# Kernel tuning notes

Measured on AMD Instinct MI355X. Metric: run time of the kernel, lower is better.

Reference implementation:

```python
import jax, jax.numpy as jnp
import numpy as np

N = 50000
E = 500000
HID = 64
HEADS = 4
LAYERS = 4
CDIM = 8


def _p(key, shape, scale=0.05):
    return jax.random.normal(key, shape, dtype=jnp.float32) * scale


def setup_inputs() -> dict:
    key = jax.random.key(0)
    ks = jax.random.split(key, 32)
    x = jax.random.normal(ks[0], (N, 8), dtype=jnp.float32)
    src = jax.random.randint(ks[1], (E,), 0, N)
    dst = jax.random.randint(ks[2], (E,), 0, N)
    edge_index = jnp.stack([src, dst]).astype(jnp.int64)
    HC = HEADS * HID
    inp = {
        "x": x,
        "edge_index": edge_index,
        # encoder: Linear(8,64), ELU, Linear(64,64), ELU
        "enc_w1": _p(ks[3], (HID, 8)), "enc_b1": _p(ks[4], (HID,)),
        "enc_w2": _p(ks[5], (HID, HID)), "enc_b2": _p(ks[6], (HID,)),
        # per-layer TransformerConv params, stacked over layers
        "Wq": _p(ks[7], (LAYERS, HC, HID)), "bq": _p(ks[8], (LAYERS, HC)),
        "Wk": _p(ks[9], (LAYERS, HC, HID)), "bk": _p(ks[10], (LAYERS, HC)),
        "Wv": _p(ks[11], (LAYERS, HC, HID)), "bv": _p(ks[12], (LAYERS, HC)),
        "Ws": _p(ks[13], (LAYERS, HID, HID)), "bs": _p(ks[14], (LAYERS, HID)),
        # output MLP: 64->64->32->8
        "out_w1": _p(ks[15], (64, HID)), "out_b1": _p(ks[16], (64,)),
        "out_w2": _p(ks[17], (32, 64)), "out_b2": _p(ks[18], (32,)),
        "out_w3": _p(ks[19], (CDIM, 32)), "out_b3": _p(ks[20], (CDIM,)),
    }
    return inp


def transformer_conv(h, src, dst, Wq, bq, Wk, bk, Wv, bv, Ws, bs):
    """PyG TransformerConv, concat=False, root_weight=True, eval mode (no dropout)."""
    n = h.shape[0]
    q = (h @ Wq.T + bq).reshape(n, HEADS, HID)
    k = (h @ Wk.T + bk).reshape(n, HEADS, HID)
    v = (h @ Wv.T + bv).reshape(n, HEADS, HID)
    # per-edge multi-head scores: (E, H)
    alpha = jnp.einsum("ehd,ehd->eh", q[dst], k[src]) / np.sqrt(HID).astype(np.float32)
    # segment softmax over edges grouped by destination node
    amax = jax.ops.segment_max(alpha, dst, num_segments=n)          # (N, H)
    ex = jnp.exp(alpha - amax[dst])                                 # (E, H)
    denom = jax.ops.segment_sum(ex, dst, num_segments=n)           # (N, H)
    w = ex / denom[dst]                                             # (E, H)
    msg = v[src] * w[:, :, None]                                    # (E, H, C)
    agg = jax.ops.segment_sum(msg, dst, num_segments=n)            # (N, H, C)
    out = agg.mean(axis=1)                                          # concat=False -> head mean
    return out + h @ Ws.T + bs                                      # skip connection


def reference(x, edge_index, enc_w1, enc_b1, enc_w2, enc_b2,
              Wq, bq, Wk, bk, Wv, bv, Ws, bs,
              out_w1, out_b1, out_w2, out_b2, out_w3, out_b3):
    src, dst = edge_index[0], edge_index[1]
    elu = jax.nn.elu
    h = elu(x @ enc_w1.T + enc_b1)
    h = elu(h @ enc_w2.T + enc_b2)
    for l in range(LAYERS):
        h = elu(transformer_conv(h, src, dst, Wq[l], bq[l], Wk[l], bk[l],
                                 Wv[l], bv[l], Ws[l], bs[l]))
        # dropout is identity in eval mode
    o = elu(h @ out_w1.T + out_b1)
    o = elu(o @ out_w2.T + out_b2)
    o = o @ out_w3.T + out_b3
    return o
```

## Files before the change

### kernel.cpp

```cpp
#include <hip/hip_runtime.h>
#include <hip/hip_bf16.h>

#define N_NODES 50000
#define N_EDGES 500000
constexpr int HID = 64;
constexpr int HC  = 256;

typedef unsigned short u16;
typedef unsigned char u8;
typedef __attribute__((ext_vector_type(8))) __bf16 bf16x8;
typedef __attribute__((ext_vector_type(4))) float f32x4;
typedef __attribute__((ext_vector_type(2))) float f32x2;

__device__ __forceinline__ float b2f(u16 u) {
    union { unsigned int i; float f; } c; c.i = ((unsigned int)u) << 16; return c.f;
}
__device__ __forceinline__ u16 f2b(float f) {
    union { float f; unsigned int i; } c; c.f = f;
    unsigned int x = c.i;
    unsigned int lsb = (x >> 16) & 1u;
    x += 0x7fffu + lsb;
    return (u16)(x >> 16);
}
__device__ __forceinline__ float elu_f(float x) { return x > 0.f ? x : expm1f(x); }


__global__ __launch_bounds__(256) void init_kernel(int* __restrict__ cnt, int* __restrict__ cursor) {
    int i = blockIdx.x * 256 + threadIdx.x;
    if (i < N_NODES) { cnt[i] = 0; cursor[i] = 0; }
}

__global__ __launch_bounds__(256) void detect_kernel(const int* __restrict__ ei, int* __restrict__ flag) {
    __shared__ int s[4];
    int t = threadIdx.x;
    int nz = ei[2 * t + 1] != 0;
    unsigned long long m = __ballot(nz);
    if ((t & 63) == 0) s[t >> 6] = (m != 0ull) ? 1 : 0;
    __syncthreads();
    if (t == 0) flag[0] = s[0] | s[1] | s[2] | s[3];
}

__global__ __launch_bounds__(256) void wcvt_kernel(const float* __restrict__ Wq, const float* __restrict__ Wk,
                                                   const float* __restrict__ Wv, const float* __restrict__ Wsk,
                                                   u16* __restrict__ w16) {
    int i = blockIdx.x * 256 + threadIdx.x;
    if (i >= 53248) return;
    const float* src; int off;
    if (i < 16384)      { src = Wq;  off = i; }
    else if (i < 32768) { src = Wk;  off = i - 16384; }
    else if (i < 49152) { src = Wv;  off = i - 32768; }
    else                { src = Wsk; off = i - 49152; }
    float4 v = ((const float4*)src)[off];
    ushort4 u; u.x = f2b(v.x); u.y = f2b(v.y); u.z = f2b(v.z); u.w = f2b(v.w);
    ((ushort4*)w16)[i] = u;
}

__global__ __launch_bounds__(256) void hist_kernel(const int* __restrict__ ei, const int* __restrict__ flag,
                                                   int* __restrict__ cnt) {
    int e = blockIdx.x * 256 + threadIdx.x;
    if (e < N_EDGES) {
        int d = flag[0] ? ei[N_EDGES + e] : ei[2 * N_EDGES + 2 * e];
        atomicAdd(&cnt[d], 1);
    }
}

__global__ __launch_bounds__(512) void scan1_kernel(const int* __restrict__ cnt,
                                                    int* __restrict__ row_start, int* __restrict__ bsum) {
    __shared__ int sc[512];
    int t = threadIdx.x;
    int i = blockIdx.x * 512 + t;
    int v = (i < N_NODES) ? cnt[i] : 0;
    sc[t] = v;
    __syncthreads();
    for (int off = 1; off < 512; off <<= 1) {
        int u = (t >= off) ? sc[t - off] : 0;
        __syncthreads();
        sc[t] += u;
        __syncthreads();
    }
    if (i < N_NODES) row_start[i] = sc[t] - v;
    if (t == 511) bsum[blockIdx.x] = sc[511];
}

__global__ __launch_bounds__(128) void scan2_kernel(int* __restrict__ bsum, int* __restrict__ row_start) {
    __shared__ int sc[128];
    const int NB = (N_NODES + 511) / 512;
    int t = threadIdx.x;
    int v = (t < NB) ? bsum[t] : 0;
    sc[t] = v;
    __syncthreads();
    for (int off = 1; off < 128; off <<= 1) {
        int u = (t >= off) ? sc[t - off] : 0;
        __syncthreads();
        sc[t] += u;
        __syncthreads();
    }
    if (t < NB) bsum[t] = sc[t] - v;
    if (t == 127) row_start[N_NODES] = sc[127];
}

__global__ __launch_bounds__(512) void scan3_kernel(int* __restrict__ row_start, const int* __restrict__ bsum) {
    int i = blockIdx.x * 512 + threadIdx.x;
    if (i < N_NODES) row_start[i] += bsum[blockIdx.x];
}

__global__ __launch_bounds__(256) void scatter_kernel(const int* __restrict__ ei, const int* __restrict__ flag,
                                const int* __restrict__ row_start, int* __restrict__ cursor,
                                int* __restrict__ csr_src) {
    int e = blockIdx.x * 256 + threadIdx.x;
    if (e < N_EDGES) {
        int isI32 = flag[0];
        int s = isI32 ? ei[e] : ei[2 * e];
        int d = isI32 ? ei[N_EDGES + e] : ei[2 * N_EDGES + 2 * e];
        int pos = row_start[d] + atomicAdd(&cursor[d], 1);
        csr_src[pos] = s;
    }
}

__global__ __launch_bounds__(256) void encoder_kernel(const float* __restrict__ x,
                               const float* __restrict__ w1, const float* __restrict__ b1,
                               const float* __restrict__ w2, const float* __restrict__ b2,
                               float* __restrict__ h) {
    __shared__ float xs[64 * 9];
    __shared__ float w1s[64 * 9];
    __shared__ u16 t1s[64 * 72];
    __shared__ u16 w2s[64 * 72];
    __shared__ float b1s[64], b2s[64];
    int t = threadIdx.x;
    int m0 = blockIdx.x * 64;

    if (t < 128) {
        int row = t >> 1, c = (t & 1) * 4;
        float4 val = make_float4(0.f, 0.f, 0.f, 0.f);
        if (m0 + row < N_NODES) val = *(const float4*)(x + (size_t)(m0 + row) * 8 + c);
        *(float4*)&xs[row * 9 + c] = val;
    }
    if (t >= 128 && t < 256) {
        int p = t - 128;
        int row = p >> 1, c = (p & 1) * 4;
        float4 val = *(const float4*)(w1 + row * 8 + c);
        *(float4*)&w1s[row * 9 + c] = val;
    }
    #pragma unroll
    for (int r = 0; r < 4; ++r) {
        int p = t + r * 256; int row = p >> 4, kc = (p & 15) * 4;
        float4 val = *(const float4*)(w2 + row * 64 + kc);
        ushort4 u; u.x = f2b(val.x); u.y = f2b(val.y); u.z = f2b(val.z); u.w = f2b(val.w);
        *(ushort4*)&w2s[row * 72 + kc] = u;
    }
    if (t < 64) { b1s[t] = b1[t]; b2s[t] = b2[t]; }
    __syncthreads();

    {
        int j = t & 63, sub = t >> 6;
        #pragma unroll
        for (int g = 0; g < 16; ++g) {
            int node = g * 4 + sub;
            float acc = b1s[j];
            #pragma unroll
            for (int m = 0; m < 8; ++m) acc += xs[node * 9 + m] * w1s[j * 9 + m];
            t1s[node * 72 + j] = f2b(elu_f(acc));
        }
    }
    __syncthreads();

    int wave = t >> 6, lane = t & 63;
    int lrow = lane & 15, quad = lane >> 4;
    int m_off = wave * 16;
    bf16x8 a0 = *(const bf16x8*)&t1s[(m_off + lrow) * 72 + quad * 8];
    bf16x8 a1 = *(const bf16x8*)&t1s[(m_off + lrow) * 72 + 32 + quad * 8];
    #pragma unroll
    for (int nsub = 0; nsub < 4; ++nsub) {
        bf16x8 b0 = *(const bf16x8*)&w2s[(nsub * 16 + lrow) * 72 + quad * 8];
        bf16x8 b1v = *(const bf16x8*)&w2s[(nsub * 16 + lrow) * 72 + 32 + quad * 8];
        f32x4 acc = {0.f, 0.f, 0.f, 0.f};
        acc = __builtin_amdgcn_mfma_f32_16x16x32_bf16(a0, b0, acc, 0, 0, 0);
        acc = __builtin_amdgcn_mfma_f32_16x16x32_bf16(a1, b1v, acc, 0, 0, 0);
        int col = nsub * 16 + lrow;
        float bias = b2s[col];
        #pragma unroll
        for (int r = 0; r < 4; ++r) {
            int row = m0 + m_off + quad * 4 + r;
            if (row < N_NODES) h[(size_t)row * 64 + col] = elu_f(acc[r] + bias);
        }
    }
}

__global__ __launch_bounds__(256) void proj_kernel(const float* __restrict__ h,
    const u16* __restrict__ wq16, const u16* __restrict__ wk16,
    const u16* __restrict__ wv16, const u16* __restrict__ wsk16,
    const float* __restrict__ bq, const float* __restrict__ bk,
    const float* __restrict__ bv, const float* __restrict__ bsk,
    int layer,
    u16* __restrict__ q, u8* __restrict__ kv, float* __restrict__ skip)
{
    __shared__ u16 as_tile[64 * 72];
    __shared__ u16 ws_tile[64 * 72];
    __shared__ float pool[64 * 68];
    u16* qst  = (u16*)pool;
    u8*  kvst = (u8*)pool;
    float* skst = pool;

    int t = threadIdx.x;
    int m0 = blockIdx.x * 64;

    #pragma unroll
    for (int r = 0; r < 4; ++r) {
        int p = t + r * 256; int row = p >> 4, kc = (p & 15) * 4;
        float4 val = make_float4(0.f, 0.f, 0.f, 0.f);
        if (m0 + row < N_NODES) val = *(const float4*)(h + (size_t)(m0 + row) * 64 + kc);
        ushort4 u; u.x = f2b(val.x); u.y = f2b(val.y); u.z = f2b(val.z); u.w = f2b(val.w);
        *(ushort4*)&as_tile[row * 72 + kc] = u;
    }
    __syncthreads();

    int wave = t >> 6, lane = t & 63;
    int lrow = lane & 15, quad = lane >> 4;
    bf16x8 a0 = *(const bf16x8*)&as_tile[(wave * 16 + lrow) * 72 + quad * 8];
    bf16x8 a1 = *(const bf16x8*)&as_tile[(wave * 16 + lrow) * 72 + 32 + quad * 8];

    const u16* Wq16  = wq16  + (size_t)layer * HC * HID;
    const u16* Wk16  = wk16  + (size_t)layer * HC * HID;
    const u16* Wv16  = wv16  + (size_t)layer * HC * HID;
    const u16* Wsk16 = wsk16 + (size_t)layer * HID * HID;
    const float* bqL  = bq  + layer * HC;
    const float* bkL  = bk  + layer * HC;
    const float* bvL  = bv  + layer * HC;
    const float* bskL = bsk + layer * HID;

    int nl = wave * 16 + lrow;
    int grow_l = m0 + nl;

    for (int ct = 0; ct < 4; ++ct) {
        int cbase = ct * 64;
        __syncthreads();
        #pragma unroll
        for (int it = 0; it < 2; ++it) {
            int p = t + it * 256; int row = p >> 3, kc = (p & 7) * 8;
            *(uint4*)&ws_tile[row * 72 + kc] = *(const uint4*)(Wq16 + (size_t)(cbase + row) * 64 + kc);
        }
        __syncthreads();
        #pragma unroll
        for (int nsub = 0; nsub < 4; ++nsub) {
            bf16x8 w0 = *(const bf16x8*)&ws_tile[(nsub * 16 + lrow) * 72 + quad * 8];
            bf16x8 w1 = *(const bf16x8*)&ws_tile[(nsub * 16 + lrow) * 72 + 32 + quad * 8];
            f32x4 acc = {0.f, 0.f, 0.f, 0.f};
            acc = __builtin_amdgcn_mfma_f32_16x16x32_bf16(w0, a0, acc, 0, 0, 0);
            acc = __builtin_amdgcn_mfma_f32_16x16x32_bf16(w1, a1, acc, 0, 0, 0);
            float4 b4 = *(const float4*)(bqL + cbase + nsub * 16 + quad * 4);
            ushort4 o;
            o.x = f2b(acc[0] + b4.x); o.y = f2b(acc[1] + b4.y);
            o.z = f2b(acc[2] + b4.z); o.w = f2b(acc[3] + b4.w);
            *(ushort4*)&qst[nl * 72 + nsub * 16 + quad * 4] = o;
        }
        __syncthreads();
        #pragma unroll
        for (int it = 0; it < 2; ++it) {
            int p = t + it * 256; int row = p >> 3, ch = p & 7;
            int grow = m0 + row;
            if (grow < N_NODES)
                *(uint4*)(q + (size_t)grow * 256 + cbase + ch * 8) = *(const uint4*)&qst[row * 72 + ch * 8];
        }
    }

    for (int ct = 0; ct < 4; ++ct) {
        int cbase = ct * 64;
        __syncthreads();
        #pragma unroll
        for (int it = 0; it < 2; ++it) {
            int p = t + it * 256; int row = p >> 3, kc = (p & 7) * 8;
            *(uint4*)&ws_tile[row * 72 + kc] = *(const uint4*)(Wk16 + (size_t)(cbase + row) * 64 + kc);
        }
        __syncthreads();
        #pragma unroll
        for (int nsub = 0; nsub < 4; ++nsub) {
            bf16x8 w0 = *(const bf16x8*)&ws_tile[(nsub * 16 + lrow) * 72 + quad * 8];
            bf16x8 w1 = *(const bf16x8*)&ws_tile[(nsub * 16 + lrow) * 72 + 32 + quad * 8];
            f32x4 acc = {0.f, 0.f, 0.f, 0.f};
            acc = __builtin_amdgcn_mfma_f32_16x16x32_bf16(w0, a0, acc, 0, 0, 0);
            acc = __builtin_amdgcn_mfma_f32_16x16x32_bf16(w1, a1, acc, 0, 0, 0);
            float4 b4 = *(const float4*)(bkL + cbase + nsub * 16 + quad * 4);
            float f0 = (acc[0] + b4.x) * 16.f, f1 = (acc[1] + b4.y) * 16.f;
            float f2v = (acc[2] + b4.z) * 16.f, f3v = (acc[3] + b4.w) * 16.f;
            int pk = __builtin_amdgcn_cvt_pk_fp8_f32(f0, f1, 0, false);
            pk = __builtin_amdgcn_cvt_pk_fp8_f32(f2v, f3v, pk, true);
            int g = nsub * 4 + quad;
            *(unsigned int*)&kvst[nl * 144 + g * 8] = (unsigned int)pk;
        }
        __syncthreads();
        #pragma unroll
        for (int it = 0; it < 2; ++it) {
            int p = t + it * 256; int row = p >> 3, kc = (p & 7) * 8;
            *(uint4*)&ws_tile[row * 72 + kc] = *(const uint4*)(Wv16 + (size_t)(cbase + row) * 64 + kc);
        }
        __syncthreads();
        #pragma unroll
        for (int nsub = 0; nsub < 4; ++nsub) {
            bf16x8 w0 = *(const bf16x8*)&ws_tile[(nsub * 16 + lrow) * 72 + quad * 8];
            bf16x8 w1 = *(const bf16x8*)&ws_tile[(nsub * 16 + lrow) * 72 + 32 + quad * 8];
            f32x4 acc = {0.f, 0.f, 0.f, 0.f};
            acc = __builtin_amdgcn_mfma_f32_16x16x32_bf16(w0, a0, acc, 0, 0, 0);
            acc = __builtin_amdgcn_mfma_f32_16x16x32_bf16(w1, a1, acc, 0, 0, 0);
            float4 b4 = *(const float4*)(bvL + cbase + nsub * 16 + quad * 4);
            float f0 = (acc[0] + b4.x) * 16.f, f1 = (acc[1] + b4.y) * 16.f;
            float f2v = (acc[2] + b4.z) * 16.f, f3v = (acc[3] + b4.w) * 16.f;
            int pk = __builtin_amdgcn_cvt_pk_fp8_f32(f0, f1, 0, false);
            pk = __builtin_amdgcn_cvt_pk_fp8_f32(f2v, f3v, pk, true);
            int g = nsub * 4 + quad;
            *(unsigned int*)&kvst[nl * 144 + g * 8 + 4] = (unsigned int)pk;
        }
        __syncthreads();
        #pragma unroll
        for (int it = 0; it < 2; ++it) {
            int p = t + it * 256; int row = p >> 3, ch = p & 7;
            int grow = m0 + row;
            if (grow < N_NODES)
                *(uint4*)(kv + (size_t)grow * 512 + cbase * 2 + ch * 16) = *(const uint4*)&kvst[row * 144 + ch * 16];
        }
    }

    {
        __syncthreads();
        #pragma unroll
        for (int it = 0; it < 2; ++it) {
            int p = t + it * 256; int row = p >> 3, kc = (p & 7) * 8;
            *(uint4*)&ws_tile[row * 72 + kc] = *(const uint4*)(Wsk16 + (size_t)row * 64 + kc);
        }
        __syncthreads();
        #pragma unroll
        for (int nsub = 0; nsub < 4; ++nsub) {
            bf16x8 w0 = *(const bf16x8*)&ws_tile[(nsub * 16 + lrow) * 72 + quad * 8];
            bf16x8 w1 = *(const bf16x8*)&ws_tile[(nsub * 16 + lrow) * 72 + 32 + quad * 8];
            f32x4 acc = {0.f, 0.f, 0.f, 0.f};
            acc = __builtin_amdgcn_mfma_f32_16x16x32_bf16(w0, a0, acc, 0, 0, 0);
            acc = __builtin_amdgcn_mfma_f32_16x16x32_bf16(w1, a1, acc, 0, 0, 0);
            float4 b4 = *(const float4*)(bskL + nsub * 16 + quad * 4);
            float4 o;
            o.x = acc[0] + b4.x; o.y = acc[1] + b4.y;
            o.z = acc[2] + b4.z; o.w = acc[3] + b4.w;
            *(float4*)&skst[nl * 68 + nsub * 16 + quad * 4] = o;
        }
        __syncthreads();
        int row = t >> 2, c0 = (t & 3) * 16;
        int grow = m0 + row;
        if (grow < N_NODES) {
            #pragma unroll
            for (int j = 0; j < 4; ++j)
                *(float4*)(skip + (size_t)grow * 64 + c0 + j * 4) = *(const float4*)&skst[row * 68 + c0 + j * 4];
        }
    }
}

__global__ __launch_bounds__(256) void attn_kernel(
    const u16* __restrict__ q, const u8* __restrict__ kv,
    const float* __restrict__ skip,
    const int* __restrict__ row_start, const int* __restrict__ csr_src,
    float* __restrict__ hout)
{
    int wave = threadIdx.x >> 6;
    int lane = threadIdx.x & 63;
    int n = blockIdx.x * 4 + wave;
    if (n >= N_NODES) return;
    ushort4 q4 = ((const ushort4*)(q + (size_t)n * 256))[lane];
    float qf0 = b2f(q4.x), qf1 = b2f(q4.y), qf2 = b2f(q4.z), qf3 = b2f(q4.w);
    const u8* kvl = kv + lane * 8;
    float l = 0.f;
    float a0 = 0.f, a1 = 0.f, a2 = 0.f, a3 = 0.f;
    int e0 = row_start[n], e1 = row_start[n + 1];
    for (int e = e0; e < e1; e += 4) {
        int rem = e1 - e;
        int i1 = rem > 1 ? e + 1 : e;
        int i2 = rem > 2 ? e + 2 : e;
        int i3 = rem > 3 ? e + 3 : e;
        int s0 = csr_src[e], s1 = csr_src[i1], s2 = csr_src[i2], s3 = csr_src[i3];
        uint2 c0 = *(const uint2*)(kvl + (size_t)s0 * 512);
        uint2 c1 = *(const uint2*)(kvl + (size_t)s1 * 512);
        uint2 c2 = *(const uint2*)(kvl + (size_t)s2 * 512);
        uint2 c3 = *(const uint2*)(kvl + (size_t)s3 * 512);
        f32x2 k0a = __builtin_amdgcn_cvt_pk_f32_fp8(c0.x, false), k0b = __builtin_amdgcn_cvt_pk_f32_fp8(c0.x, true);
        f32x2 k1a = __builtin_amdgcn_cvt_pk_f32_fp8(c1.x, false), k1b = __builtin_amdgcn_cvt_pk_f32_fp8(c1.x, true);
        f32x2 k2a = __builtin_amdgcn_cvt_pk_f32_fp8(c2.x, false), k2b = __builtin_amdgcn_cvt_pk_f32_fp8(c2.x, true);
        f32x2 k3a = __builtin_amdgcn_cvt_pk_f32_fp8(c3.x, false), k3b = __builtin_amdgcn_cvt_pk_f32_fp8(c3.x, true);
        float p0 = qf0 * k0a.x + qf1 * k0a.y + qf2 * k0b.x + qf3 * k0b.y;
        float p1 = qf0 * k1a.x + qf1 * k1a.y + qf2 * k1b.x + qf3 * k1b.y;
        float p2 = qf0 * k2a.x + qf1 * k2a.y + qf2 * k2b.x + qf3 * k2b.y;
        float p3 = qf0 * k3a.x + qf1 * k3a.y + qf2 * k3b.x + qf3 * k3b.y;
        p0 += __shfl_xor(p0, 1); p1 += __shfl_xor(p1, 1); p2 += __shfl_xor(p2, 1); p3 += __shfl_xor(p3, 1);
        p0 += __shfl_xor(p0, 2); p1 += __shfl_xor(p1, 2); p2 += __shfl_xor(p2, 2); p3 += __shfl_xor(p3, 2);
        p0 += __shfl_xor(p0, 4); p1 += __shfl_xor(p1, 4); p2 += __shfl_xor(p2, 4); p3 += __shfl_xor(p3, 4);
        p0 += __shfl_xor(p0, 8); p1 += __shfl_xor(p1, 8); p2 += __shfl_xor(p2, 8); p3 += __shfl_xor(p3, 8);
        const float S = 0.0078125f;
        float w0 = __expf(p0 * S);
        float w1 = rem > 1 ? __expf(p1 * S) : 0.f;
        float w2 = rem > 2 ? __expf(p2 * S) : 0.f;
        float w3 = rem > 3 ? __expf(p3 * S) : 0.f;
        l += (w0 + w1) + (w2 + w3);
        f32x2 v0a = __builtin_amdgcn_cvt_pk_f32_fp8(c0.y, false), v0b = __builtin_amdgcn_cvt_pk_f32_fp8(c0.y, true);
        f32x2 v1a = __builtin_amdgcn_cvt_pk_f32_fp8(c1.y, false), v1b = __builtin_amdgcn_cvt_pk_f32_fp8(c1.y, true);
        f32x2 v2a = __builtin_amdgcn_cvt_pk_f32_fp8(c2.y, false), v2b = __builtin_amdgcn_cvt_pk_f32_fp8(c2.y, true);
        f32x2 v3a = __builtin_amdgcn_cvt_pk_f32_fp8(c3.y, false), v3b = __builtin_amdgcn_cvt_pk_f32_fp8(c3.y, true);
        a0 += w0 * v0a.x + w1 * v1a.x + w2 * v2a.x + w3 * v3a.x;
        a1 += w0 * v0a.y + w1 * v1a.y + w2 * v2a.y + w3 * v3a.y;
        a2 += w0 * v0b.x + w1 * v1b.x + w2 * v2b.x + w3 * v3b.x;
        a3 += w0 * v0b.y + w1 * v1b.y + w2 * v2b.y + w3 * v3b.y;
    }
    float inv = l > 0.f ? 1.f / l : 0.f;
    a0 *= inv; a1 *= inv; a2 *= inv; a3 *= inv;
    a0 += __shfl_xor(a0, 16); a0 += __shfl_xor(a0, 32);
    a1 += __shfl_xor(a1, 16); a1 += __shfl_xor(a1, 32);
    a2 += __shfl_xor(a2, 16); a2 += __shfl_xor(a2, 32);
    a3 += __shfl_xor(a3, 16); a3 += __shfl_xor(a3, 32);
    if ((lane >> 4) == 0) {
        const float OS = 0.015625f;
        float4 sk = ((const float4*)(skip + (size_t)n * 64))[lane];
        float4 o;
        o.x = elu_f(OS * a0 + sk.x);
        o.y = elu_f(OS * a1 + sk.y);
        o.z = elu_f(OS * a2 + sk.z);
        o.w = elu_f(OS * a3 + sk.w);
        ((float4*)(hout + (size_t)n * 64))[lane] = o;
    }
}

__global__ __launch_bounds__(256) void mlp_kernel(const float* __restrict__ h,
    const float* __restrict__ w1, const float* __restrict__ b1,
    const float* __restrict__ w2, const float* __restrict__ b2,
    const float* __restrict__ w3, const float* __restrict__ b3,
    float* __restrict__ out)
{
    __shared__ u16 hs[64 * 72];
    __shared__ u16 w1s[64 * 72];
    __shared__ u16 t1s[64 * 72];
    __shared__ u16 w2s[32 * 72];
    __shared__ float t2s[64 * 33];
    __shared__ float w3s[8 * 33];
    __shared__ float b1s[64], b2s[32], b3s[8];
    int t = threadIdx.x;
    int m0 = blockIdx.x * 64;

    #pragma unroll
    for (int r = 0; r < 4; ++r) {
        int p = t + r * 256; int row = p >> 4, kc = (p & 15) * 4;
        float4 val = make_float4(0.f, 0.f, 0.f, 0.f);
        if (m0 + row < N_NODES) val = *(const float4*)(h + (size_t)(m0 + row) * 64 + kc);
        ushort4 u; u.x = f2b(val.x); u.y = f2b(val.y); u.z = f2b(val.z); u.w = f2b(val.w);
        *(ushort4*)&hs[row * 72 + kc] = u;
    }
    #pragma unroll
    for (int r = 0; r < 4; ++r) {
        int p = t + r * 256; int row = p >> 4, kc = (p & 15) * 4;
        float4 val = *(const float4*)(w1 + row * 64 + kc);
        ushort4 u; u.x = f2b(val.x); u.y = f2b(val.y); u.z = f2b(val.z); u.w = f2b(val.w);
        *(ushort4*)&w1s[row * 72 + kc] = u;
    }
    #pragma unroll
    for (int r = 0; r < 2; ++r) {
        int p = t + r * 256; int row = p >> 4, kc = (p & 15) * 4;
        float4 val = *(const float4*)(w2 + row * 64 + kc);
        ushort4 u; u.x = f2b(val.x); u.y = f2b(val.y); u.z = f2b(val.z); u.w = f2b(val.w);
        *(ushort4*)&w2s[row * 72 + kc] = u;
    }
    if (t < 8 * 32) { int r = t >> 5, c = t & 31; w3s[r * 33 + c] = w3[t]; }
    if (t < 64) b1s[t] = b1[t];
    if (t >= 64 && t < 96) b2s[t - 64] = b2[t - 64];
    if (t >= 96 && t < 104) b3s[t - 96] = b3[t - 96];
    __syncthreads();

    int wave = t >> 6, lane = t & 63;
    int lrow = lane & 15, quad = lane >> 4;
    int m_off = wave * 16;

    {
        bf16x8 a0 = *(const bf16x8*)&hs[(m_off + lrow) * 72 + quad * 8];
        bf16x8 a1 = *(const bf16x8*)&hs[(m_off + lrow) * 72 + 32 + quad * 8];
        #pragma unroll
        for (int nsub = 0; nsub < 4; ++nsub) {
            bf16x8 b0 = *(const bf16x8*)&w1s[(nsub * 16 + lrow) * 72 + quad * 8];
            bf16x8 b1v = *(const bf16x8*)&w1s[(nsub * 16 + lrow) * 72 + 32 + quad * 8];
            f32x4 acc = {0.f, 0.f, 0.f, 0.f};
            acc = __builtin_amdgcn_mfma_f32_16x16x32_bf16(a0, b0, acc, 0, 0, 0);
            acc = __builtin_amdgcn_mfma_f32_16x16x32_bf16(a1, b1v, acc, 0, 0, 0);
            int col = nsub * 16 + lrow;
            float bias = b1s[col];
            #pragma unroll
            for (int r = 0; r < 4; ++r) {
                int row = m_off + quad * 4 + r;
                t1s[row * 72 + col] = f2b(elu_f(acc[r] + bias));
            }
        }
    }
    __syncthreads();

    {
        bf16x8 a0 = *(const bf16x8*)&t1s[(m_off + lrow) * 72 + quad * 8];
        bf16x8 a1 = *(const bf16x8*)&t1s[(m_off + lrow) * 72 + 32 + quad * 8];
        #pragma unroll
        for (int nsub = 0; nsub < 2; ++nsub) {
            bf16x8 b0 = *(const bf16x8*)&w2s[(nsub * 16 + lrow) * 72 + quad * 8];
            bf16x8 b1v = *(const bf16x8*)&w2s[(nsub * 16 + lrow) * 72 + 32 + quad * 8];
            f32x4 acc = {0.f, 0.f, 0.f, 0.f};
            acc = __builtin_amdgcn_mfma_f32_16x16x32_bf16(a0, b0, acc, 0, 0, 0);
            acc = __builtin_amdgcn_mfma_f32_16x16x32_bf16(a1, b1v, acc, 0, 0, 0);
            int col = nsub * 16 + lrow;
            float bias = b2s[col];
            #pragma unroll
            for (int r = 0; r < 4; ++r) {
                int row = m_off + quad * 4 + r;
                t2s[row * 33 + col] = elu_f(acc[r] + bias);
            }
        }
    }
    __syncthreads();

    #pragma unroll
    for (int r = 0; r < 2; ++r) {
        int idx = t + r * 256;
        int node = idx >> 3, j = idx & 7;
        int row = m0 + node;
        if (row < N_NODES) {
            float acc = b3s[j];
            #pragma unroll
            for (int kk = 0; kk < 32; ++kk) acc += t2s[node * 33 + kk] * w3s[j * 33 + kk];
            out[(size_t)row * 8 + j] = acc;
        }
    }
}

extern "C" void kernel_launch(void* const* d_in, const int* in_sizes, int n_in,
                              void* d_out, int out_size, void* d_ws, size_t ws_size,
                              hipStream_t stream) {
    (void)in_sizes; (void)n_in; (void)out_size; (void)ws_size;
    const float* x   = (const float*)d_in[0];
    const int* ei    = (const int*)d_in[1];
    const float* ew1 = (const float*)d_in[2];
    const float* eb1 = (const float*)d_in[3];
    const float* ew2 = (const float*)d_in[4];
    const float* eb2 = (const float*)d_in[5];
    const float* Wq  = (const float*)d_in[6];
    const float* bq  = (const float*)d_in[7];
    const float* Wk  = (const float*)d_in[8];
    const float* bk  = (const float*)d_in[9];
    const float* Wv  = (const float*)d_in[10];
    const float* bv  = (const float*)d_in[11];
    const float* Wsk = (const float*)d_in[12];
    const float* bsk = (const float*)d_in[13];
    const float* ow1 = (const float*)d_in[14];
    const float* ob1 = (const float*)d_in[15];
    const float* ow2 = (const float*)d_in[16];
    const float* ob2 = (const float*)d_in[17];
    const float* ow3 = (const float*)d_in[18];
    const float* ob3 = (const float*)d_in[19];

    char* ws = (char*)d_ws;
    size_t off = 0;
    auto alloc = [&](size_t bytes) -> void* {
        void* p = ws + off;
        off += (bytes + 255) & ~(size_t)255;
        return p;
    };
    float* h0    = (float*)alloc((size_t)N_NODES * 64 * 4);
    float* h1    = (float*)alloc((size_t)N_NODES * 64 * 4);
    u16*   q     = (u16*)  alloc((size_t)N_NODES * 256 * 2);
    u8*    kv    = (u8*)   alloc((size_t)N_NODES * 512);
    float* skp   = (float*)alloc((size_t)N_NODES * 64 * 4);
    u16*   w16   = (u16*)  alloc((size_t)212992 * 2);
    int*   cnt   = (int*)  alloc((size_t)N_NODES * 4);
    int*   cursor= (int*)  alloc((size_t)N_NODES * 4);
    int*   rowst = (int*)  alloc((size_t)(N_NODES + 1) * 4);
    int*   csr   = (int*)  alloc((size_t)N_EDGES * 4);
    int*   bsum  = (int*)  alloc(512);
    int*   flag  = (int*)  alloc(256);

    u16* wq16  = w16;
    u16* wk16  = w16 + 65536;
    u16* wv16  = w16 + 131072;
    u16* wsk16 = w16 + 196608;

    const int NB = (N_NODES + 511) / 512;

    init_kernel<<<(N_NODES + 255) / 256, 256, 0, stream>>>(cnt, cursor);
    detect_kernel<<<1, 256, 0, stream>>>(ei, flag);
    wcvt_kernel<<<208, 256, 0, stream>>>(Wq, Wk, Wv, Wsk, w16);
    hist_kernel<<<(N_EDGES + 255) / 256, 256, 0, stream>>>(ei, flag, cnt);
    scan1_kernel<<<NB, 512, 0, stream>>>(cnt, rowst, bsum);
    scan2_kernel<<<1, 128, 0, stream>>>(bsum, rowst);
    scan3_kernel<<<NB, 512, 0, stream>>>(rowst, bsum);
    scatter_kernel<<<(N_EDGES + 255) / 256, 256, 0, stream>>>(ei, flag, rowst, cursor, csr);

    encoder_kernel<<<(N_NODES + 63) / 64, 256, 0, stream>>>(x, ew1, eb1, ew2, eb2, h0);

    float* hin = h0;
    float* hout = h1;
    for (int l = 0; l < 4; ++l) {
        proj_kernel<<<(N_NODES + 63) / 64, 256, 0, stream>>>(hin, wq16, wk16, wv16, wsk16,
                                                             bq, bk, bv, bsk, l, q, kv, skp);
        attn_kernel<<<(N_NODES + 3) / 4, 256, 0, stream>>>(q, kv, skp, rowst, csr, hout);
        float* tmp = hin; hin = hout; hout = tmp;
    }

    mlp_kernel<<<(N_NODES + 63) / 64, 256, 0, stream>>>(hin, ow1, ob1, ow2, ob2, ow3, ob3, (float*)d_out);
}
```

Measured before the change: 471.5 us.

## Prefetch weight tiles in projection loop and simplify attention edge loads

The projection kernel's separate Q, K, V and skip loops are merged into one 13-step loop that loads the next weight tile from global memory into registers while the current tile is being used, hiding global-load latency behind the MFMA work. The attention kernel folds the 1/sqrt scale and log2(e) into q once and uses exp2f, which removes a multiply per score. It also pads the CSR array with 8 zeroed entries so tail-edge index loads no longer need clamping. The unified loop adds mode branches and holds prefetch registers, and padded indices read node 0's kv even though those weights are masked to zero.

Result: slower. 491.8 us (+4.3%).

```diff
diff --git a/kernel.cpp b/kernel.cpp
--- a/kernel.cpp
+++ b/kernel.cpp
@@ -25,9 +25,11 @@
 __device__ __forceinline__ float elu_f(float x) { return x > 0.f ? x : expm1f(x); }
 
 
-__global__ __launch_bounds__(256) void init_kernel(int* __restrict__ cnt, int* __restrict__ cursor) {
+__global__ __launch_bounds__(256) void init_kernel(int* __restrict__ cnt, int* __restrict__ cursor,
+                                                   int* __restrict__ csr) {
     int i = blockIdx.x * 256 + threadIdx.x;
     if (i < N_NODES) { cnt[i] = 0; cursor[i] = 0; }
+    if (blockIdx.x == 0 && threadIdx.x < 8) csr[N_EDGES + threadIdx.x] = 0;
 }
 
 __global__ __launch_bounds__(256) void detect_kernel(const int* __restrict__ ei, int* __restrict__ flag) {
@@ -229,17 +231,42 @@
     const float* bskL = bsk + layer * HID;
 
     int nl = wave * 16 + lrow;
-    int grow_l = m0 + nl;
-
-    for (int ct = 0; ct < 4; ++ct) {
-        int cbase = ct * 64;
+
+    auto tile_base = [&](int idx) -> const u16* {
+        if (idx < 4) return Wq16 + (size_t)(idx * 64) * 64;
+        if (idx < 12) {
+            int p2 = idx - 4; int ctk = p2 >> 1;
+            return ((p2 & 1) ? Wv16 : Wk16) + (size_t)(ctk * 64) * 64;
+        }
+        return Wsk16;
+    };
+
+    int p0 = t, p1 = t + 256;
+    int g_off0 = (p0 >> 3) * 64 + (p0 & 7) * 8;
+    int g_off1 = (p1 >> 3) * 64 + (p1 & 7) * 8;
+    int l_off0 = (p0 >> 3) * 72 + (p0 & 7) * 8;
+    int l_off1 = (p1 >> 3) * 72 + (p1 & 7) * 8;
+
+    uint4 pre0 = *(const uint4*)(tile_base(0) + g_off0);
+    uint4 pre1 = *(const uint4*)(tile_base(0) + g_off1);
+
+    for (int idx = 0; idx < 13; ++idx) {
+        const float* bt; int cbase; int mode;
+        if (idx < 4)       { bt = bqL + idx * 64; cbase = idx * 64; mode = 0; }
+        else if (idx < 12) { int p2 = idx - 4; int ctk = p2 >> 1; cbase = ctk * 64;
+                             if ((p2 & 1) == 0) { bt = bkL + cbase; mode = 1; }
+                             else               { bt = bvL + cbase; mode = 2; } }
+        else               { bt = bskL; cbase = 0; mode = 3; }
+
         __syncthreads();
-        #pragma unroll
-        for (int it = 0; it < 2; ++it) {
-            int p = t + it * 256; int row = p >> 3, kc = (p & 7) * 8;
-            *(uint4*)&ws_tile[row * 72 + kc] = *(const uint4*)(Wq16 + (size_t)(cbase + row) * 64 + kc);
+        *(uint4*)&ws_tile[l_off0] = pre0;
+        *(uint4*)&ws_tile[l_off1] = pre1;
+        if (idx + 1 < 13) {
+            pre0 = *(const uint4*)(tile_base(idx + 1) + g_off0);
+            pre1 = *(const uint4*)(tile_base(idx + 1) + g_off1);
         }
         __syncthreads();
+
         #pragma unroll
         for (int nsub = 0; nsub < 4; ++nsub) {
             bf16x8 w0 = *(const bf16x8*)&ws_tile[(nsub * 16 + lrow) * 72 + quad * 8];
@@ -247,106 +274,54 @@
             f32x4 acc = {0.f, 0.f, 0.f, 0.f};
             acc = __builtin_amdgcn_mfma_f32_16x16x32_bf16(w0, a0, acc, 0, 0, 0);
             acc = __builtin_amdgcn_mfma_f32_16x16x32_bf16(w1, a1, acc, 0, 0, 0);
-            float4 b4 = *(const float4*)(bqL + cbase + nsub * 16 + quad * 4);
-            ushort4 o;
-            o.x = f2b(acc[0] + b4.x); o.y = f2b(acc[1] + b4.y);
-            o.z = f2b(acc[2] + b4.z); o.w = f2b(acc[3] + b4.w);
-            *(ushort4*)&qst[nl * 72 + nsub * 16 + quad * 4] = o;
-        }
-        __syncthreads();
-        #pragma unroll
-        for (int it = 0; it < 2; ++it) {
-            int p = t + it * 256; int row = p >> 3, ch = p & 7;
+            float4 b4 = *(const float4*)(bt + nsub * 16 + quad * 4);
+            if (mode == 0) {
+                ushort4 o;
+                o.x = f2b(acc[0] + b4.x); o.y = f2b(acc[1] + b4.y);
+                o.z = f2b(acc[2] + b4.z); o.w = f2b(acc[3] + b4.w);
+                *(ushort4*)&qst[nl * 72 + nsub * 16 + quad * 4] = o;
+            } else if (mode == 1 || mode == 2) {
+                float f0 = (acc[0] + b4.x) * 16.f, f1 = (acc[1] + b4.y) * 16.f;
+                float f2v = (acc[2] + b4.z) * 16.f, f3v = (acc[3] + b4.w) * 16.f;
+                int pk = __builtin_amdgcn_cvt_pk_fp8_f32(f0, f1, 0, false);
+                pk = __builtin_amdgcn_cvt_pk_fp8_f32(f2v, f3v, pk, true);
+                int g = nsub * 4 + quad;
+                *(unsigned int*)&kvst[nl * 144 + g * 8 + (mode == 2 ? 4 : 0)] = (unsigned int)pk;
+            } else {
+                float4 o;
+                o.x = acc[0] + b4.x; o.y = acc[1] + b4.y;
+                o.z = acc[2] + b4.z; o.w = acc[3] + b4.w;
+                *(float4*)&skst[nl * 68 + nsub * 16 + quad * 4] = o;
+            }
+        }
+
+        if (mode == 0) {
+            __syncthreads();
+            #pragma unroll
+            for (int it = 0; it < 2; ++it) {
+                int p = t + it * 256; int row = p >> 3, ch = p & 7;
+                int grow = m0 + row;
+                if (grow < N_NODES)
+                    *(uint4*)(q + (size_t)grow * 256 + cbase + ch * 8) = *(const uint4*)&qst[row * 72 + ch * 8];
+            }
+        } else if (mode == 2) {
+            __syncthreads();
+            #pragma unroll
+            for (int it = 0; it < 2; ++it) {
+                int p = t + it * 256; int row = p >> 3, ch = p & 7;
+                int grow = m0 + row;
+                if (grow < N_NODES)
+                    *(uint4*)(kv + (size_t)grow * 512 + cbase * 2 + ch * 16) = *(const uint4*)&kvst[row * 144 + ch * 16];
+            }
+        } else if (mode == 3) {
+            __syncthreads();
+            int row = t >> 2, c0 = (t & 3) * 16;
             int grow = m0 + row;
-            if (grow < N_NODES)
-                *(uint4*)(q + (size_t)grow * 256 + cbase + ch * 8) = *(const uint4*)&qst[row * 72 + ch * 8];
-        }
-    }
-
-    for (int ct = 0; ct < 4; ++ct) {
-        int cbase = ct * 64;
-        __syncthreads();
-        #pragma unroll
-        for (int it = 0; it < 2; ++it) {
-            int p = t + it * 256; int row = p >> 3, kc = (p & 7) * 8;
-            *(uint4*)&ws_tile[row * 72 + kc] = *(const uint4*)(Wk16 + (size_t)(cbase + row) * 64 + kc);
-        }
-        __syncthreads();
-        #pragma unroll
-        for (int nsub = 0; nsub < 4; ++nsub) {
-            bf16x8 w0 = *(const bf16x8*)&ws_tile[(nsub * 16 + lrow) * 72 + quad * 8];
-            bf16x8 w1 = *(const bf16x8*)&ws_tile[(nsub * 16 + lrow) * 72 + 32 + quad * 8];
-            f32x4 acc = {0.f, 0.f, 0.f, 0.f};
-            acc = __builtin_amdgcn_mfma_f32_16x16x32_bf16(w0, a0, acc, 0, 0, 0);
-            acc = __builtin_amdgcn_mfma_f32_16x16x32_bf16(w1, a1, acc, 0, 0, 0);
-            float4 b4 = *(const float4*)(bkL + cbase + nsub * 16 + quad * 4);
-            float f0 = (acc[0] + b4.x) * 16.f, f1 = (acc[1] + b4.y) * 16.f;
-            float f2v = (acc[2] + b4.z) * 16.f, f3v = (acc[3] + b4.w) * 16.f;
-            int pk = __builtin_amdgcn_cvt_pk_fp8_f32(f0, f1, 0, false);
-            pk = __builtin_amdgcn_cvt_pk_fp8_f32(f2v, f3v, pk, true);
-            int g = nsub * 4 + quad;
-            *(unsigned int*)&kvst[nl * 144 + g * 8] = (unsigned int)pk;
-        }
-        __syncthreads();
-        #pragma unroll
-        for (int it = 0; it < 2; ++it) {
-            int p = t + it * 256; int row = p >> 3, kc = (p & 7) * 8;
-            *(uint4*)&ws_tile[row * 72 + kc] = *(const uint4*)(Wv16 + (size_t)(cbase + row) * 64 + kc);
-        }
-        __syncthreads();
-        #pragma unroll
-        for (int nsub = 0; nsub < 4; ++nsub) {
-            bf16x8 w0 = *(const bf16x8*)&ws_tile[(nsub * 16 + lrow) * 72 + quad * 8];
-            bf16x8 w1 = *(const bf16x8*)&ws_tile[(nsub * 16 + lrow) * 72 + 32 + quad * 8];
-            f32x4 acc = {0.f, 0.f, 0.f, 0.f};
-            acc = __builtin_amdgcn_mfma_f32_16x16x32_bf16(w0, a0, acc, 0, 0, 0);
-            acc = __builtin_amdgcn_mfma_f32_16x16x32_bf16(w1, a1, acc, 0, 0, 0);
-            float4 b4 = *(const float4*)(bvL + cbase + nsub * 16 + quad * 4);
-            float f0 = (acc[0] + b4.x) * 16.f, f1 = (acc[1] + b4.y) * 16.f;
-            float f2v = (acc[2] + b4.z) * 16.f, f3v = (acc[3] + b4.w) * 16.f;
-            int pk = __builtin_amdgcn_cvt_pk_fp8_f32(f0, f1, 0, false);
-            pk = __builtin_amdgcn_cvt_pk_fp8_f32(f2v, f3v, pk, true);
-            int g = nsub * 4 + quad;
-            *(unsigned int*)&kvst[nl * 144 + g * 8 + 4] = (unsigned int)pk;
-        }
-        __syncthreads();
-        #pragma unroll
-        for (int it = 0; it < 2; ++it) {
-            int p = t + it * 256; int row = p >> 3, ch = p & 7;
-            int grow = m0 + row;
-            if (grow < N_NODES)
-                *(uint4*)(kv + (size_t)grow * 512 + cbase * 2 + ch * 16) = *(const uint4*)&kvst[row * 144 + ch * 16];
-        }
-    }
-
-    {
-        __syncthreads();
-        #pragma unroll
-        for (int it = 0; it < 2; ++it) {
-            int p = t + it * 256; int row = p >> 3, kc = (p & 7) * 8;
-            *(uint4*)&ws_tile[row * 72 + kc] = *(const uint4*)(Wsk16 + (size_t)row * 64 + kc);
-        }
-        __syncthreads();
-        #pragma unroll
-        for (int nsub = 0; nsub < 4; ++nsub) {
-            bf16x8 w0 = *(const bf16x8*)&ws_tile[(nsub * 16 + lrow) * 72 + quad * 8];
-            bf16x8 w1 = *(const bf16x8*)&ws_tile[(nsub * 16 + lrow) * 72 + 32 + quad * 8];
-            f32x4 acc = {0.f, 0.f, 0.f, 0.f};
-            acc = __builtin_amdgcn_mfma_f32_16x16x32_bf16(w0, a0, acc, 0, 0, 0);
-            acc = __builtin_amdgcn_mfma_f32_16x16x32_bf16(w1, a1, acc, 0, 0, 0);
-            float4 b4 = *(const float4*)(bskL + nsub * 16 + quad * 4);
-            float4 o;
-            o.x = acc[0] + b4.x; o.y = acc[1] + b4.y;
-            o.z = acc[2] + b4.z; o.w = acc[3] + b4.w;
-            *(float4*)&skst[nl * 68 + nsub * 16 + quad * 4] = o;
-        }
-        __syncthreads();
-        int row = t >> 2, c0 = (t & 3) * 16;
-        int grow = m0 + row;
-        if (grow < N_NODES) {
-            #pragma unroll
-            for (int j = 0; j < 4; ++j)
-                *(float4*)(skip + (size_t)grow * 64 + c0 + j * 4) = *(const float4*)&skst[row * 68 + c0 + j * 4];
+            if (grow < N_NODES) {
+                #pragma unroll
+                for (int j = 0; j < 4; ++j)
+                    *(float4*)(skip + (size_t)grow * 64 + c0 + j * 4) = *(const float4*)&skst[row * 68 + c0 + j * 4];
+            }
         }
     }
 }
@@ -361,18 +336,16 @@
     int lane = threadIdx.x & 63;
     int n = blockIdx.x * 4 + wave;
     if (n >= N_NODES) return;
+    const float SC = 0.0078125f * 1.44269504f;
     ushort4 q4 = ((const ushort4*)(q + (size_t)n * 256))[lane];
-    float qf0 = b2f(q4.x), qf1 = b2f(q4.y), qf2 = b2f(q4.z), qf3 = b2f(q4.w);
+    float qf0 = b2f(q4.x) * SC, qf1 = b2f(q4.y) * SC, qf2 = b2f(q4.z) * SC, qf3 = b2f(q4.w) * SC;
     const u8* kvl = kv + lane * 8;
     float l = 0.f;
     float a0 = 0.f, a1 = 0.f, a2 = 0.f, a3 = 0.f;
     int e0 = row_start[n], e1 = row_start[n + 1];
     for (int e = e0; e < e1; e += 4) {
         int rem = e1 - e;
-        int i1 = rem > 1 ? e + 1 : e;
-        int i2 = rem > 2 ? e + 2 : e;
-        int i3 = rem > 3 ? e + 3 : e;
-        int s0 = csr_src[e], s1 = csr_src[i1], s2 = csr_src[i2], s3 = csr_src[i3];
+        int s0 = csr_src[e], s1 = csr_src[e + 1], s2 = csr_src[e + 2], s3 = csr_src[e + 3];
         uint2 c0 = *(const uint2*)(kvl + (size_t)s0 * 512);
         uint2 c1 = *(const uint2*)(kvl + (size_t)s1 * 512);
         uint2 c2 = *(const uint2*)(kvl + (size_t)s2 * 512);
@@ -389,11 +362,10 @@
         p0 += __shfl_xor(p0, 2); p1 += __shfl_xor(p1, 2); p2 += __shfl_xor(p2, 2); p3 += __shfl_xor(p3, 2);
         p0 += __shfl_xor(p0, 4); p1 += __shfl_xor(p1, 4); p2 += __shfl_xor(p2, 4); p3 += __shfl_xor(p3, 4);
         p0 += __shfl_xor(p0, 8); p1 += __shfl_xor(p1, 8); p2 += __shfl_xor(p2, 8); p3 += __shfl_xor(p3, 8);
-        const float S = 0.0078125f;
-        float w0 = __expf(p0 * S);
-        float w1 = rem > 1 ? __expf(p1 * S) : 0.f;
-        float w2 = rem > 2 ? __expf(p2 * S) : 0.f;
-        float w3 = rem > 3 ? __expf(p3 * S) : 0.f;
+        float w0 = exp2f(p0);
+        float w1 = rem > 1 ? exp2f(p1) : 0.f;
+        float w2 = rem > 2 ? exp2f(p2) : 0.f;
+        float w3 = rem > 3 ? exp2f(p3) : 0.f;
         l += (w0 + w1) + (w2 + w3);
         f32x2 v0a = __builtin_amdgcn_cvt_pk_f32_fp8(c0.y, false), v0b = __builtin_amdgcn_cvt_pk_f32_fp8(c0.y, true);
         f32x2 v1a = __builtin_amdgcn_cvt_pk_f32_fp8(c1.y, false), v1b = __builtin_amdgcn_cvt_pk_f32_fp8(c1.y, true);
@@ -567,7 +539,7 @@
     int*   cnt   = (int*)  alloc((size_t)N_NODES * 4);
     int*   cursor= (int*)  alloc((size_t)N_NODES * 4);
     int*   rowst = (int*)  alloc((size_t)(N_NODES + 1) * 4);
-    int*   csr   = (int*)  alloc((size_t)N_EDGES * 4);
+    int*   csr   = (int*)  alloc((size_t)(N_EDGES + 8) * 4);
     int*   bsum  = (int*)  alloc(512);
     int*   flag  = (int*)  alloc(256);
 
@@ -578,7 +550,7 @@
 
     const int NB = (N_NODES + 511) / 512;
 
-    init_kernel<<<(N_NODES + 255) / 256, 256, 0, stream>>>(cnt, cursor);
+    init_kernel<<<(N_NODES + 255) / 256, 256, 0, stream>>>(cnt, cursor, csr);
     detect_kernel<<<1, 256, 0, stream>>>(ei, flag);
     wcvt_kernel<<<208, 256, 0, stream>>>(Wq, Wk, Wv, Wsk, w16);
     hist_kernel<<<(N_EDGES + 255) / 256, 256, 0, stream>>>(ei, flag, cnt);
```
